# Optimization experiments

Hardware: AMD Instinct MI355X
Metric: run time of the kernel (lower is better)

The kernel has to match this reference:

```python
import jax, jax.numpy as jnp
import numpy as np
from jax import lax

EPS = 1e-5
C, H, W, G = 512, 32, 32, 32


def instance_norm(x):
    # torch InstanceNorm2d: affine=False, biased variance over (H,W)
    mu = x.mean(axis=(2, 3), keepdims=True)
    var = ((x - mu) ** 2).mean(axis=(2, 3), keepdims=True)
    return (x - mu) / jnp.sqrt(var + EPS)


def conv2d(x, w, stride=1, padding=0, groups=1, lhs_dilation=None):
    return lax.conv_general_dilated(
        x, w, (stride, stride), [(padding, padding)] * 2,
        lhs_dilation=lhs_dilation, feature_group_count=groups,
        dimension_numbers=('NCHW', 'OIHW', 'NCHW'))


def leaky_relu(x):
    return jnp.where(x >= 0, x, 0.2 * x)


def unfold(img, k, s):
    # img: (C,H,W) -> (nH*nW, C, k, k); matches torch unfold(1,k,s).unfold(2,k,s)
    c, h, w = img.shape
    nH = (h - k) // s + 1
    nW = (w - k) // s + 1
    rows = []
    for i in range(k):
        cols = [img[:, i:i + s * (nH - 1) + 1:s, j:j + s * (nW - 1) + 1:s] for j in range(k)]
        rows.append(jnp.stack(cols, axis=-1))  # (C,nH,nW,k)
    p = jnp.stack(rows, axis=-2)  # (C,nH,nW,k,k)
    return p.transpose(1, 2, 0, 3, 4).reshape(nH * nW, c, k, k)


def ral(bg, fg, rate=2, ksize=3, scale=10.0):
    # Region Affinity Layer (contextual-attention style), batch = 1
    b, c, h, w = fg.shape
    fh, fw = h // rate, w // rate
    # bilinear downsample by exactly 2 (half-pixel) == 2x2 average pooling
    fg_small = fg.reshape(b, c, fh, rate, fw, rate).mean(axis=(3, 5))
    bk = 2 * rate
    bg_patches = unfold(jnp.pad(bg, ((0, 0), (0, 0), (1, 1), (1, 1)))[0], bk, rate)      # (256,C,4,4)
    fg_patches = unfold(jnp.pad(fg_small, ((0, 0), (0, 0), (1, 1), (1, 1)))[0], ksize, 1)  # (256,C,3,3)
    norm = jnp.sqrt((fg_patches ** 2).sum(axis=(1, 2, 3), keepdims=True))
    fgp_n = fg_patches / jnp.maximum(norm, 1e-4)
    score = conv2d(fg_small, fgp_n, padding=1)        # (1,256,16,16)
    attn = jax.nn.softmax(score * scale, axis=1)
    # conv_transpose2d(attn, bg_patches, stride=rate, padding=1) via lhs dilation
    w_t = jnp.flip(bg_patches, axis=(-2, -1)).transpose(1, 0, 2, 3)  # (C,256,4,4)
    return conv2d(attn, w_t, padding=bk - 2, lhs_dilation=(rate, rate)) / 4.0  # (1,C,32,32)


def forward(x, gus, w_sk3, b_sk3, w_sk5, b_sk5, w_sk7, b_sk7,
            w_fc, b_fc, w_fc0, b_fc0, w_fc1, b_fc1, w_fc2, b_fc2, w_down, w_fuse):
    # ---- SKConv (M=3 branches: k=3/5/7, groups=32) ----
    feas = []
    for wgt, bias, pad in ((w_sk3, b_sk3, 1), (w_sk5, b_sk5, 2), (w_sk7, b_sk7, 3)):
        f = conv2d(x, wgt, padding=pad, groups=G) + bias[None, :, None, None]
        feas.append(jax.nn.relu(instance_norm(f)))
    feas = jnp.stack(feas, axis=1)                # (B,3,C,H,W)
    fea_s = feas.sum(axis=1).mean(axis=(2, 3))    # (B,C) global pool
    fea_z = fea_s @ w_fc.T + b_fc                 # (B,32)
    att = jnp.stack([fea_z @ w_fc0.T + b_fc0,
                     fea_z @ w_fc1.T + b_fc1,
                     fea_z @ w_fc2.T + b_fc2], axis=1)  # (B,3,C)
    att = jax.nn.softmax(att, axis=1)[..., None, None]
    out_32 = (feas * att).sum(axis=1)             # (1,C,32,32)
    out_res = out_32
    out_32 = ral(out_32, out_32)
    b, c, h, w = out_32.shape
    # ---- gaussian-weighted broadcast sum: (P,H,W)x(C,H,W)->(P,C)->raw reshape ----
    gus_out = jnp.einsum('pxy,cxy->pc', gus, out_32[0]).reshape(b, c, h, w)
    # ---- CSA patch correlation ----
    csa2_in = jax.nn.sigmoid(out_32)
    p_fff = unfold(jnp.pad(out_32, ((0, 0), (0, 0), (1, 1), (1, 1)))[0], 3, 1)    # (1024,C,3,3)
    p_f = unfold(jnp.pad(csa2_in, ((0, 0), (0, 0), (1, 1), (1, 1)))[0], 3, 1)     # (1024,C,3,3)
    p_conv = unfold(csa2_in[0], 1, 1)                                             # (1024,C,1,1)
    csa_a = (p_conv * p_f).mean(axis=1)                                           # (1024,3,3)
    csa_a = jax.nn.softmax(csa_a.reshape(h * w, 9), axis=1).reshape(h * w, 1, 3, 3)
    out_csa = (csa_a * p_fff).sum(axis=(-2, -1)).reshape(b, c, h, w)
    # ---- fuse ----
    z = jnp.concatenate([gus_out, out_csa], axis=1)       # (1,1024,32,32)
    z = leaky_relu(instance_norm(conv2d(z, w_down)))
    z = jnp.concatenate([z, out_res], axis=1)             # (1,1024,32,32)
    return leaky_relu(instance_norm(conv2d(z, w_fuse)))   # (1,512,32,32)


def _gaussian_buffer():
    # util.gussin(1.5): gaussian centered at every grid position of a 32x32 map
    v = 1.5
    r = np.arange(32)
    i, k, x, y = np.meshgrid(r, r, r, r, indexing='ij')
    g = np.exp(-((x - i) ** 2 + (y - k) ** 2) / (2 * v * v)) / (2 * np.pi * v * v)
    return jnp.asarray(g.reshape(32 * 32, 32, 32), dtype=jnp.float32)


def setup_inputs():
    key = jax.random.key(0)
    ks = jax.random.split(key, 12)
    s = 0.02
    return {
        'x': jax.random.normal(ks[0], (1, C, H, W), jnp.float32),
        'gus': _gaussian_buffer(),
        'w_sk3': jax.random.normal(ks[1], (C, C // G, 3, 3), jnp.float32) * s,
        'b_sk3': jnp.zeros((C,), jnp.float32),
        'w_sk5': jax.random.normal(ks[2], (C, C // G, 5, 5), jnp.float32) * s,
        'b_sk5': jnp.zeros((C,), jnp.float32),
        'w_sk7': jax.random.normal(ks[3], (C, C // G, 7, 7), jnp.float32) * s,
        'b_sk7': jnp.zeros((C,), jnp.float32),
        'w_fc': jax.random.normal(ks[4], (32, C), jnp.float32) * s,
        'b_fc': jnp.zeros((32,), jnp.float32),
        'w_fc0': jax.random.normal(ks[5], (C, 32), jnp.float32) * s,
        'b_fc0': jnp.zeros((C,), jnp.float32),
        'w_fc1': jax.random.normal(ks[6], (C, 32), jnp.float32) * s,
        'b_fc1': jnp.zeros((C,), jnp.float32),
        'w_fc2': jax.random.normal(ks[7], (C, 32), jnp.float32) * s,
        'b_fc2': jnp.zeros((C,), jnp.float32),
        'w_down': jax.random.normal(ks[8], (512, 1024, 1, 1), jnp.float32) * s,
        'w_fuse': jax.random.normal(ks[9], (512, 1024, 1, 1), jnp.float32) * s,
    }


def reference(x, gus, w_sk3, b_sk3, w_sk5, b_sk5, w_sk7, b_sk7, w_fc, b_fc,
              w_fc0, b_fc0, w_fc1, b_fc1, w_fc2, b_fc2, w_down, w_fuse):
    return forward(x, gus, w_sk3, b_sk3, w_sk5, b_sk5, w_sk7, b_sk7,
                   w_fc, b_fc, w_fc0, b_fc0, w_fc1, b_fc1, w_fc2, b_fc2,
                   w_down, w_fuse)
```

## Files before the change

kernel.cpp:

```cpp
#include <hip/hip_runtime.h>
#include <math.h>

#define EPSN 1e-5f

typedef __attribute__((ext_vector_type(8))) short bf16x8;
typedef __attribute__((ext_vector_type(4))) float f32x4;

__device__ __forceinline__ ushort f2bf(float f) {
  unsigned u = __float_as_uint(f);
  unsigned r = (u + 0x7fff + ((u >> 16) & 1)) >> 16;
  return (ushort)r;
}

__device__ __forceinline__ void breduce2(float& a, float& b, float* lds) {
#pragma unroll
  for (int o = 32; o > 0; o >>= 1) {
    a += __shfl_down(a, o);
    b += __shfl_down(b, o);
  }
  int lane = threadIdx.x & 63, wid = threadIdx.x >> 6;
  __syncthreads();
  if (lane == 0) { lds[wid] = a; lds[4 + wid] = b; }
  __syncthreads();
  a = lds[0] + lds[1] + lds[2] + lds[3];
  b = lds[4] + lds[5] + lds[6] + lds[7];
}

__device__ __forceinline__ float breduce_sum(float v, float* lds) {
#pragma unroll
  for (int o = 32; o > 0; o >>= 1) v += __shfl_down(v, o);
  int lane = threadIdx.x & 63, wid = threadIdx.x >> 6;
  __syncthreads();
  if (lane == 0) lds[wid] = v;
  __syncthreads();
  return lds[0] + lds[1] + lds[2] + lds[3];
}

__device__ __forceinline__ float breduce_max(float v, float* lds) {
#pragma unroll
  for (int o = 32; o > 0; o >>= 1) v = fmaxf(v, __shfl_down(v, o));
  int lane = threadIdx.x & 63, wid = threadIdx.x >> 6;
  __syncthreads();
  if (lane == 0) lds[wid] = v;
  __syncthreads();
  return fmaxf(fmaxf(lds[0], lds[1]), fmaxf(lds[2], lds[3]));
}

__global__ void pre_kernel(const float* __restrict__ gus,
                           const float* __restrict__ wdown,
                           const float* __restrict__ wfuse,
                           ushort* __restrict__ gus_bf,
                           ushort* __restrict__ wdown_bf,
                           ushort* __restrict__ wfuse_bf,
                           ushort* __restrict__ resd) {
  int bid = blockIdx.x, tid = threadIdx.x;
  if (bid < 2048) {
    int i = bid * 1024 + tid * 4;
    const float* src; ushort* dst; int off;
    if (i < 1048576) { src = gus; dst = gus_bf; off = i; }
    else if (i < 1572864) { src = wdown; dst = wdown_bf; off = i - 1048576; }
    else { src = wfuse; dst = wfuse_bf; off = i - 1572864; }
    float4 v = *(const float4*)&src[off];
    ushort4 o = {f2bf(v.x), f2bf(v.y), f2bf(v.z), f2bf(v.w)};
    *(ushort4*)&dst[off] = o;
  } else {
    int t8 = (bid - 2048) * 256 + tid;
    uint4 z = {0u, 0u, 0u, 0u};
#pragma unroll
    for (int k = 0; k < 4; ++k) *(uint4*)&resd[(size_t)(t8 + k * 65536) * 8] = z;
  }
}

__device__ __forceinline__ void finish3(float a[2][4], float bv, int m, int c,
                                        int y0, int xb, float* feas,
                                        float* bmean, float* red) {
  int tid = threadIdx.x, lane = tid & 63, wid = tid >> 6, pr = wid >> 1;
  float s = 0.f, ss = 0.f;
#pragma unroll
  for (int rr = 0; rr < 2; ++rr)
#pragma unroll
    for (int px = 0; px < 4; ++px) {
      a[rr][px] += bv;
      s += a[rr][px];
      ss += a[rr][px] * a[rr][px];
    }
#pragma unroll
  for (int o = 32; o > 0; o >>= 1) {
    s += __shfl_down(s, o);
    ss += __shfl_down(ss, o);
  }
  __syncthreads();
  if (lane == 0) { red[wid] = s; red[4 + wid] = ss; }
  __syncthreads();
  s = red[2 * pr] + red[2 * pr + 1];
  ss = red[4 + 2 * pr] + red[4 + 2 * pr + 1];
  float mean = s * (1.f / 1024.f);
  float var = ss * (1.f / 1024.f) - mean * mean;
  float inv = rsqrtf(var + EPSN);
  float rs = 0.f;
#pragma unroll
  for (int rr = 0; rr < 2; ++rr) {
    float4 o4;
    float* ov = (float*)&o4;
#pragma unroll
    for (int px = 0; px < 4; ++px) {
      float v = (a[rr][px] - mean) * inv;
      v = v > 0.f ? v : 0.f;
      ov[px] = v;
      rs += v;
    }
    *(float4*)&feas[(size_t)(m * 512 + c) * 1024 + (y0 + rr) * 32 + xb] = o4;
  }
#pragma unroll
  for (int o = 32; o > 0; o >>= 1) rs += __shfl_down(rs, o);
  __syncthreads();
  if (lane == 0) red[wid] = rs;
  __syncthreads();
  if ((tid & 127) == 0)
    bmean[m * 512 + c] = (red[2 * pr] + red[2 * pr + 1]) * (1.f / 1024.f);
}

__global__ __launch_bounds__(256) void sk_all5(
    const float* __restrict__ x, const float* __restrict__ w3,
    const float* __restrict__ b3, const float* __restrict__ w5,
    const float* __restrict__ b5, const float* __restrict__ w7,
    const float* __restrict__ b7, float* __restrict__ feas,
    float* __restrict__ bmean) {
  __shared__ float chanp[8 * 1536];
  __shared__ float ws7p[2 * 16 * 56];
  __shared__ float ws5p[2 * 16 * 40];
  __shared__ float ws3p[2 * 16 * 12];
  __shared__ float red[8];
  int bid = blockIdx.x, tid = threadIdx.x;
  int c0 = bid * 2, g = c0 >> 4;
  for (int i = tid; i < 8 * 1536; i += 256) chanp[i] = 0.f;
  for (int i = tid; i < 1792; i += 256) {
    int cw = i / 896, rem = i - cw * 896;
    int ic = rem / 56, t = rem - ic * 56, r = t >> 3, k = t & 7;
    ws7p[i] = (r < 7 && k < 7) ? w7[(c0 + cw) * 784 + ic * 49 + r * 7 + k] : 0.f;
  }
  for (int i = tid; i < 1280; i += 256) {
    int cw = i / 640, rem = i - cw * 640;
    int ic = rem / 40, t = rem - ic * 40, r = t >> 3, k = t & 7;
    ws5p[i] = (r < 5 && k < 5) ? w5[(c0 + cw) * 400 + ic * 25 + r * 5 + k] : 0.f;
  }
  for (int i = tid; i < 384; i += 256) {
    int cw = i / 192, rem = i - cw * 192;
    int ic = rem / 12, t = rem - ic * 12, r = t >> 2, k = t & 3;
    ws3p[i] = (k < 3) ? w3[(c0 + cw) * 144 + ic * 9 + r * 3 + k] : 0.f;
  }
  int ch = tid >> 7;
  int idx = tid & 127;
  int y0 = (idx >> 3) * 2, xb = (idx & 7) * 4;
  float a7[2][4] = {}, a5[2][4] = {}, a3[2][4] = {};
  int srow = tid >> 3, scol = (tid & 7) * 4;
  for (int half = 0; half < 2; ++half) {
    __syncthreads();
#pragma unroll
    for (int j = 0; j < 8; ++j) {
      float4 xv = *(const float4*)&x[(size_t)(g * 16 + half * 8 + j) * 1024 + tid * 4];
      *(float4*)&chanp[j * 1536 + srow * 48 + 4 + scol] = xv;
    }
    __syncthreads();
    for (int cc = 0; cc < 8; ++cc) {
      int ic = half * 8 + cc;
      float sg[8][12];
#pragma unroll
      for (int s = 0; s < 8; ++s) {
        int r = y0 - 3 + s;
        if ((unsigned)r < 32u) {
          const float* rp = &chanp[cc * 1536 + r * 48 + xb];
          float4 q0 = *(const float4*)rp;
          float4 q1 = *(const float4*)(rp + 4);
          float4 q2 = *(const float4*)(rp + 8);
          sg[s][0] = q0.x; sg[s][1] = q0.y; sg[s][2] = q0.z; sg[s][3] = q0.w;
          sg[s][4] = q1.x; sg[s][5] = q1.y; sg[s][6] = q1.z; sg[s][7] = q1.w;
          sg[s][8] = q2.x; sg[s][9] = q2.y; sg[s][10] = q2.z; sg[s][11] = q2.w;
        } else {
#pragma unroll
          for (int t = 0; t < 12; ++t) sg[s][t] = 0.f;
        }
      }
      const float* W7 = &ws7p[ch * 896 + ic * 56];
      const float* W5 = &ws5p[ch * 640 + ic * 40];
      const float* W3 = &ws3p[ch * 192 + ic * 12];
#pragma unroll
      for (int dy = 0; dy < 7; ++dy) {
        float4 wa = *(const float4*)(W7 + dy * 8);
        float4 wb = *(const float4*)(W7 + dy * 8 + 4);
        float wv[7] = {wa.x, wa.y, wa.z, wa.w, wb.x, wb.y, wb.z};
#pragma unroll
        for (int kx = 0; kx < 7; ++kx)
#pragma unroll
          for (int px = 0; px < 4; ++px) {
            a7[0][px] += sg[dy][px + kx + 1] * wv[kx];
            a7[1][px] += sg[dy + 1][px + kx + 1] * wv[kx];
          }
      }
#pragma unroll
      for (int d5 = 0; d5 < 5; ++d5) {
        float4 va = *(const float4*)(W5 + d5 * 8);
        float wv[5] = {va.x, va.y, va.z, va.w, W5[d5 * 8 + 4]};
#pragma unroll
        for (int kx = 0; kx < 5; ++kx)
#pragma unroll
          for (int px = 0; px < 4; ++px) {
            a5[0][px] += sg[d5 + 1][px + kx + 2] * wv[kx];
            a5[1][px] += sg[d5 + 2][px + kx + 2] * wv[kx];
          }
      }
#pragma unroll
      for (int d3 = 0; d3 < 3; ++d3) {
        float4 ta = *(const float4*)(W3 + d3 * 4);
        float wv[3] = {ta.x, ta.y, ta.z};
#pragma unroll
        for (int kx = 0; kx < 3; ++kx)
#pragma unroll
          for (int px = 0; px < 4; ++px) {
            a3[0][px] += sg[d3 + 2][px + kx + 3] * wv[kx];
            a3[1][px] += sg[d3 + 3][px + kx + 3] * wv[kx];
          }
      }
    }
  }
  int c = c0 + ch;
  finish3(a3, b3[c], 0, c, y0, xb, feas, bmean, red);
  finish3(a5, b5[c], 1, c, y0, xb, feas, bmean, red);
  finish3(a7, b7[c], 2, c, y0, xb, feas, bmean, red);
}

__global__ __launch_bounds__(256) void blend_fc(
    const float* __restrict__ feas, const float* __restrict__ bmean,
    const float* __restrict__ wfc, const float* __restrict__ bfc,
    const float* __restrict__ w0, const float* __restrict__ b0,
    const float* __restrict__ w1, const float* __restrict__ b1,
    const float* __restrict__ w2, const float* __restrict__ b2,
    float* __restrict__ res, ushort* __restrict__ Zt2,
    ushort* __restrict__ resd) {
  __shared__ float sfea[512];
  __shared__ float zpart[8][32];
  __shared__ float zz[32];
  __shared__ float lv[3][32];
  __shared__ float attb[3][32];
  __shared__ float tile[32][33];
  int tid = threadIdx.x;
  int pb = blockIdx.x * 32, cb = blockIdx.y * 32;
  for (int c = tid; c < 512; c += 256)
    sfea[c] = bmean[c] + bmean[512 + c] + bmean[1024 + c];
  __syncthreads();
  {
    int j = tid & 31, seg = tid >> 5;
    float p = 0.f;
    for (int c = seg * 64; c < seg * 64 + 64; ++c) p += sfea[c] * wfc[j * 512 + c];
    zpart[seg][j] = p;
  }
  __syncthreads();
  if (tid < 32) {
    float d = bfc[tid];
#pragma unroll
    for (int s = 0; s < 8; ++s) d += zpart[s][tid];
    zz[tid] = d;
  }
  __syncthreads();
  if (tid < 96) {
    int m = tid >> 5, cl = tid & 31;
    const float* wm = (m == 0) ? w0 : (m == 1) ? w1 : w2;
    const float* bm = (m == 0) ? b0 : (m == 1) ? b1 : b2;
    float l = bm[cb + cl];
#pragma unroll
    for (int j = 0; j < 32; ++j) l += zz[j] * wm[(cb + cl) * 32 + j];
    lv[m][cl] = l;
  }
  __syncthreads();
  if (tid < 32) {
    float l0 = lv[0][tid], l1 = lv[1][tid], l2 = lv[2][tid];
    float mx = fmaxf(l0, fmaxf(l1, l2));
    float e0 = expf(l0 - mx), e1 = expf(l1 - mx), e2 = expf(l2 - mx);
    float inv = 1.f / (e0 + e1 + e2);
    attb[0][tid] = e0 * inv; attb[1][tid] = e1 * inv; attb[2][tid] = e2 * inv;
  }
  __syncthreads();
  int tx = tid & 31, ty = tid >> 5;
  int pos = pb + tx;
  int yy = pos >> 5, xx = pos & 31;
  int ki0 = (yy + 1) & 1, pi0 = (yy + 1 - ki0) >> 1;
  int kj0 = (xx + 1) & 1, pj0 = (xx + 1 - kj0) >> 1;
#pragma unroll
  for (int r = 0; r < 4; ++r) {
    int cl = ty + r * 8;
    int c = cb + cl;
    float v = feas[c * 1024 + pos] * attb[0][cl] +
              feas[(512 + c) * 1024 + pos] * attb[1][cl] +
              feas[(1024 + c) * 1024 + pos] * attb[2][cl];
    res[c * 1024 + pos] = v;
    tile[cl][tx] = v;
    ushort bv16 = f2bf(v);
#pragma unroll
    for (int ai = 0; ai < 2; ++ai) {
      int ki = ki0 + 2 * ai, pi = pi0 - ai;
      if ((unsigned)pi >= 16u) continue;
#pragma unroll
      for (int aj = 0; aj < 2; ++aj) {
        int kj = kj0 + 2 * aj, pj = pj0 - aj;
        if ((unsigned)pj >= 16u) continue;
        resd[((size_t)(ki * 4 + kj) << 17) + (size_t)c * 256 + pi * 16 + pj] = bv16;
      }
    }
  }
  __syncthreads();
#pragma unroll
  for (int r = 0; r < 4; ++r) {
    int pl = ty + r * 8;
    Zt2[(size_t)(pb + pl) * 1024 + 512 + cb + tx] = f2bf(tile[tx][pl]);
  }
}

__global__ __launch_bounds__(256) void gram_part2(const float* __restrict__ res,
                                                  float* __restrict__ Apart) {
  __shared__ float ch[4][324];
  int tid = threadIdx.x;
  int qb = blockIdx.x * 64, pb = blockIdx.y * 64;
  int kc = blockIdx.z;
  int tx = tid & 15, ty = tid >> 4;
  for (int i = tid; i < 4 * 324; i += 256) ((float*)ch)[i] = 0.f;
  int pi = (pb + ty * 4) >> 4, pj = (pb + ty * 4) & 15;
  int qi = (qb + tx * 4) >> 4, qj = (qb + tx * 4) & 15;
  int lane = tid & 63, wv = tid >> 6;
  int sr = lane >> 2, sc = (lane & 3) * 4;
  float acc[4][4] = {};
  for (int c0 = kc * 16; c0 < kc * 16 + 16; c0 += 4) {
    __syncthreads();
    {
      const float* src = res + (size_t)(c0 + wv) * 1024 + (2 * sr) * 32 + 2 * sc;
      float4 r0a = *(const float4*)src;
      float4 r0b = *(const float4*)(src + 4);
      float4 r1a = *(const float4*)(src + 32);
      float4 r1b = *(const float4*)(src + 36);
      float* dst = &ch[wv][(sr + 1) * 18 + sc + 1];
      dst[0] = 0.25f * (r0a.x + r0a.y + r1a.x + r1a.y);
      dst[1] = 0.25f * (r0a.z + r0a.w + r1a.z + r1a.w);
      dst[2] = 0.25f * (r0b.x + r0b.y + r1b.x + r1b.y);
      dst[3] = 0.25f * (r0b.z + r0b.w + r1b.z + r1b.w);
    }
    __syncthreads();
#pragma unroll
    for (int cc = 0; cc < 4; ++cc) {
      float ps[3][6], qs[3][6];
#pragma unroll
      for (int u = 0; u < 3; ++u) {
        const float* pr = &ch[cc][(pi + u) * 18 + pj];
        const float* qr = &ch[cc][(qi + u) * 18 + qj];
#pragma unroll
        for (int t = 0; t < 6; ++t) { ps[u][t] = pr[t]; qs[u][t] = qr[t]; }
      }
#pragma unroll
      for (int u = 0; u < 3; ++u)
#pragma unroll
        for (int v = 0; v < 3; ++v)
#pragma unroll
          for (int i = 0; i < 4; ++i)
#pragma unroll
            for (int j = 0; j < 4; ++j)
              acc[i][j] += ps[u][v + i] * qs[u][v + j];
    }
  }
#pragma unroll
  for (int i = 0; i < 4; ++i) {
    float4 o4 = {acc[i][0], acc[i][1], acc[i][2], acc[i][3]};
    *(float4*)&Apart[(size_t)kc * 65536 + (pb + ty * 4 + i) * 256 + qb + tx * 4] = o4;
  }
}

__global__ __launch_bounds__(256) void attn_soft3(const float* __restrict__ Apart,
                                                  ushort* __restrict__ attnT) {
  __shared__ float red[8];
  int q = blockIdx.x, t = threadIdx.x;
  float d = 0.f, s = 0.f;
#pragma unroll
  for (int k = 0; k < 32; ++k) {
    d += Apart[(size_t)k * 65536 + t * 257];
    s += Apart[(size_t)k * 65536 + q * 256 + t];
  }
  float invn = 10.f / fmaxf(sqrtf(fmaxf(d, 0.f)), 1e-4f);
  float v = s * invn;
  float mx = breduce_max(v, red);
  float e = expf(v - mx);
  float sm = breduce_sum(e, red);
  attnT[q * 256 + t] = f2bf(e / sm);
}

__global__ __launch_bounds__(256) void mfma_tconv(const ushort* __restrict__ attnT,
                                                  const ushort* __restrict__ resd,
                                                  float* __restrict__ T) {
  int tid = threadIdx.x;
  int wv = tid >> 6, lane = tid & 63;
  int quad = lane >> 4, m16 = lane & 15;
  int nb = blockIdx.x * 64, qb = blockIdx.y * 64;
  int b = blockIdx.z;
  const ushort* Ap = attnT + (size_t)(qb + wv * 16 + m16) * 256 + quad * 8;
  const ushort* Bp = resd + (size_t)b * 131072 + (size_t)(nb + m16) * 256 + quad * 8;
  f32x4 ac0 = {0.f, 0.f, 0.f, 0.f}, ac1 = ac0, ac2 = ac0, ac3 = ac0;
#pragma unroll 2
  for (int k0 = 0; k0 < 256; k0 += 32) {
    bf16x8 af = *(const bf16x8*)(Ap + k0);
    bf16x8 b0 = *(const bf16x8*)(Bp + k0);
    bf16x8 b1 = *(const bf16x8*)(Bp + 16 * 256 + k0);
    bf16x8 b2 = *(const bf16x8*)(Bp + 32 * 256 + k0);
    bf16x8 b3 = *(const bf16x8*)(Bp + 48 * 256 + k0);
    ac0 = __builtin_amdgcn_mfma_f32_16x16x32_bf16(af, b0, ac0, 0, 0, 0);
    ac1 = __builtin_amdgcn_mfma_f32_16x16x32_bf16(af, b1, ac1, 0, 0, 0);
    ac2 = __builtin_amdgcn_mfma_f32_16x16x32_bf16(af, b2, ac2, 0, 0, 0);
    ac3 = __builtin_amdgcn_mfma_f32_16x16x32_bf16(af, b3, ac3, 0, 0, 0);
  }
  int row = qb + wv * 16 + quad * 4;
  float* Cb = T + (size_t)b * 131072;
  f32x4 accs[4] = {ac0, ac1, ac2, ac3};
#pragma unroll
  for (int nt = 0; nt < 4; ++nt)
#pragma unroll
    for (int r = 0; r < 4; ++r)
      Cb[(size_t)(row + r) * 512 + nb + nt * 16 + m16] = accs[nt][r];
}

__global__ __launch_bounds__(256) void tcomb2(const float* __restrict__ T,
                                              float* __restrict__ orlt,
                                              float* __restrict__ sigt,
                                              ushort* __restrict__ orlT) {
  __shared__ float tl[32][33];
  int nb = blockIdx.x * 32, cb = blockIdx.y * 32;
  int tx = threadIdx.x & 31, ty = threadIdx.x >> 5;
#pragma unroll
  for (int r = 0; r < 4; ++r) {
    int nl = ty + r * 8;
    int n = nb + nl, c = cb + tx;
    int y = n >> 5, x = n & 31;
    int i0 = (y + 1) >> 1, ki0 = (y + 1) & 1;
    int j0 = (x + 1) >> 1, kj0 = (x + 1) & 1;
    float sum = 0.f;
#pragma unroll
    for (int iy = 0; iy < 2; ++iy) {
      int i = i0 - iy, ki = ki0 + 2 * iy;
      if ((unsigned)i >= 16u) continue;
#pragma unroll
      for (int ix = 0; ix < 2; ++ix) {
        int j = j0 - ix, kj = kj0 + 2 * ix;
        if ((unsigned)j >= 16u) continue;
        sum += T[((ki * 4 + kj) * 256 + i * 16 + j) * 512 + c];
      }
    }
    float v = sum * 0.25f;
    orlt[n * 512 + c] = v;
    sigt[n * 512 + c] = 1.f / (1.f + expf(-v));
    tl[nl][tx] = v;
  }
  __syncthreads();
#pragma unroll
  for (int r = 0; r < 4; ++r) {
    int cl = ty + r * 8;
    orlT[(size_t)(cb + cl) * 1024 + nb + tx] = f2bf(tl[tx][cl]);
  }
}

__global__ __launch_bounds__(256) void gus_csa(
    const ushort* __restrict__ gus_bf, const ushort* __restrict__ orlT,
    const float* __restrict__ sigt, const float* __restrict__ orlt,
    ushort* __restrict__ Zt) {
  __shared__ float red[8];
  __shared__ float a9s[9];
  int tid = threadIdx.x;
  if (blockIdx.x < 128) {
    const int K = 1024;
    int wv = tid >> 6, lane = tid & 63;
    int quad = lane >> 4, m16 = lane & 15;
    int nb = (blockIdx.x & 7) * 64, mb = (blockIdx.x >> 3) * 64;
    const ushort* Ap = gus_bf + (size_t)(mb + wv * 16 + m16) * K + quad * 8;
    const ushort* Bp = orlT + (size_t)(nb + m16) * K + quad * 8;
    f32x4 ac0 = {0.f, 0.f, 0.f, 0.f}, ac1 = ac0, ac2 = ac0, ac3 = ac0;
#pragma unroll 2
    for (int k0 = 0; k0 < K; k0 += 32) {
      bf16x8 af = *(const bf16x8*)(Ap + k0);
      bf16x8 b0 = *(const bf16x8*)(Bp + k0);
      bf16x8 b1 = *(const bf16x8*)(Bp + (size_t)16 * K + k0);
      bf16x8 b2 = *(const bf16x8*)(Bp + (size_t)32 * K + k0);
      bf16x8 b3 = *(const bf16x8*)(Bp + (size_t)48 * K + k0);
      ac0 = __builtin_amdgcn_mfma_f32_16x16x32_bf16(af, b0, ac0, 0, 0, 0);
      ac1 = __builtin_amdgcn_mfma_f32_16x16x32_bf16(af, b1, ac1, 0, 0, 0);
      ac2 = __builtin_amdgcn_mfma_f32_16x16x32_bf16(af, b2, ac2, 0, 0, 0);
      ac3 = __builtin_amdgcn_mfma_f32_16x16x32_bf16(af, b3, ac3, 0, 0, 0);
    }
    int row = mb + wv * 16 + quad * 4;
    f32x4 accs[4] = {ac0, ac1, ac2, ac3};
#pragma unroll
    for (int nt = 0; nt < 4; ++nt) {
      int c = nb + nt * 16 + m16;
#pragma unroll
      for (int r = 0; r < 4; ++r) {
        int p = row + r;
        int pos = ((p & 1) << 9) + c;
        int kk = p >> 1;
        Zt[(size_t)pos * 1024 + kk] = f2bf(accs[nt][r]);
      }
    }
    return;
  }
  int n = blockIdx.x - 128;
  int ny = n >> 5, nx = n & 31;
  int c2 = tid * 2;
  float2 ctr = *(const float2*)&sigt[n * 512 + c2];
  float part[9];
#pragma unroll
  for (int u = 0; u < 3; ++u) {
    int yy = ny + u - 1;
#pragma unroll
    for (int v = 0; v < 3; ++v) {
      int xx = nx + v - 1;
      float2 nb2 = {0.f, 0.f};
      if ((unsigned)yy < 32u && (unsigned)xx < 32u)
        nb2 = *(const float2*)&sigt[(yy * 32 + xx) * 512 + c2];
      part[u * 3 + v] = ctr.x * nb2.x + ctr.y * nb2.y;
    }
  }
  float a[9];
#pragma unroll
  for (int t = 0; t < 9; ++t) a[t] = breduce_sum(part[t], red) * (1.f / 512.f);
  float mx = a[0];
#pragma unroll
  for (int t = 1; t < 9; ++t) mx = fmaxf(mx, a[t]);
  float sum = 0.f;
#pragma unroll
  for (int t = 0; t < 9; ++t) { a[t] = expf(a[t] - mx); sum += a[t]; }
  if (tid == 0) {
    float inv = 1.f / sum;
#pragma unroll
    for (int t = 0; t < 9; ++t) a9s[t] = a[t] * inv;
  }
  __syncthreads();
  float2 acc = {0.f, 0.f};
#pragma unroll
  for (int u = 0; u < 3; ++u) {
    int yy = ny + u - 1;
#pragma unroll
    for (int v = 0; v < 3; ++v) {
      int xx = nx + v - 1;
      if ((unsigned)yy < 32u && (unsigned)xx < 32u) {
        float w = a9s[u * 3 + v];
        float2 ov = *(const float2*)&orlt[(yy * 32 + xx) * 512 + c2];
        acc.x += w * ov.x;
        acc.y += w * ov.y;
      }
    }
  }
  int kk = 512 + (n >> 1);
  int pos0 = ((n & 1) << 9) + c2;
  Zt[(size_t)pos0 * 1024 + kk] = f2bf(acc.x);
  Zt[(size_t)(pos0 + 1) * 1024 + kk] = f2bf(acc.y);
}

__global__ __launch_bounds__(256) void mfma_gemm_ks(const ushort* __restrict__ A,
                                                    const ushort* __restrict__ Bt,
                                                    float* __restrict__ Cp,
                                                    int N) {
  const int KF = 1024;
  int tid = threadIdx.x;
  int wv = tid >> 6, lane = tid & 63;
  int quad = lane >> 4, m16 = lane & 15;
  int nb = blockIdx.x * 64, mb = blockIdx.y * 64;
  int kh = blockIdx.z;
  const ushort* Ap = A + (size_t)(mb + wv * 16 + m16) * KF + kh * 512 + quad * 8;
  const ushort* Bp = Bt + (size_t)(nb + m16) * KF + kh * 512 + quad * 8;
  f32x4 ac0 = {0.f, 0.f, 0.f, 0.f}, ac1 = ac0, ac2 = ac0, ac3 = ac0;
#pragma unroll 2
  for (int k0 = 0; k0 < 512; k0 += 32) {
    bf16x8 af = *(const bf16x8*)(Ap + k0);
    bf16x8 b0 = *(const bf16x8*)(Bp + k0);
    bf16x8 b1 = *(const bf16x8*)(Bp + (size_t)16 * KF + k0);
    bf16x8 b2 = *(const bf16x8*)(Bp + (size_t)32 * KF + k0);
    bf16x8 b3 = *(const bf16x8*)(Bp + (size_t)48 * KF + k0);
    ac0 = __builtin_amdgcn_mfma_f32_16x16x32_bf16(af, b0, ac0, 0, 0, 0);
    ac1 = __builtin_amdgcn_mfma_f32_16x16x32_bf16(af, b1, ac1, 0, 0, 0);
    ac2 = __builtin_amdgcn_mfma_f32_16x16x32_bf16(af, b2, ac2, 0, 0, 0);
    ac3 = __builtin_amdgcn_mfma_f32_16x16x32_bf16(af, b3, ac3, 0, 0, 0);
  }
  int row = mb + wv * 16 + quad * 4;
  float* C = Cp + (size_t)kh * 524288;
  f32x4 accs[4] = {ac0, ac1, ac2, ac3};
#pragma unroll
  for (int nt = 0; nt < 4; ++nt)
#pragma unroll
    for (int r = 0; r < 4; ++r)
      C[(size_t)(row + r) * N + nb + nt * 16 + m16] = accs[nt][r];
}

__global__ __launch_bounds__(256) void norm_down2(const float* __restrict__ ra,
                                                  ushort* __restrict__ Zt2) {
  __shared__ float red[8];
  int c = blockIdx.x, tid = threadIdx.x;
  float v[4];
  float s = 0.f, ss = 0.f;
#pragma unroll
  for (int r = 0; r < 4; ++r) {
    int i = c * 1024 + tid + r * 256;
    v[r] = ra[i] + ra[524288 + i];
    s += v[r];
    ss += v[r] * v[r];
  }
  breduce2(s, ss, red);
  float mean = s * (1.f / 1024.f);
  float var = ss * (1.f / 1024.f) - mean * mean;
  float inv = rsqrtf(var + EPSN);
#pragma unroll
  for (int r = 0; r < 4; ++r) {
    float t = (v[r] - mean) * inv;
    t = t >= 0.f ? t : 0.2f * t;
    Zt2[(size_t)(tid + r * 256) * 1024 + c] = f2bf(t);
  }
}

__global__ __launch_bounds__(256) void norm_leaky2(const float* __restrict__ ra,
                                                   float* __restrict__ out) {
  __shared__ float red[8];
  int c = blockIdx.x, tid = threadIdx.x;
  float v[4];
  float s = 0.f, ss = 0.f;
#pragma unroll
  for (int r = 0; r < 4; ++r) {
    int i = c * 1024 + tid + r * 256;
    v[r] = ra[i] + ra[524288 + i];
    s += v[r];
    ss += v[r] * v[r];
  }
  breduce2(s, ss, red);
  float mean = s * (1.f / 1024.f);
  float var = ss * (1.f / 1024.f) - mean * mean;
  float inv = rsqrtf(var + EPSN);
#pragma unroll
  for (int r = 0; r < 4; ++r) {
    float t = (v[r] - mean) * inv;
    out[c * 1024 + tid + r * 256] = t >= 0.f ? t : 0.2f * t;
  }
}

extern "C" void kernel_launch(void* const* d_in, const int* in_sizes, int n_in,
                              void* d_out, int out_size, void* d_ws, size_t ws_size,
                              hipStream_t stream) {
  const float* x = (const float*)d_in[0];
  const float* gus = (const float*)d_in[1];
  const float* w3 = (const float*)d_in[2];
  const float* b3 = (const float*)d_in[3];
  const float* w5 = (const float*)d_in[4];
  const float* b5 = (const float*)d_in[5];
  const float* w7 = (const float*)d_in[6];
  const float* b7 = (const float*)d_in[7];
  const float* wfc = (const float*)d_in[8];
  const float* bfc = (const float*)d_in[9];
  const float* w0 = (const float*)d_in[10];
  const float* b0 = (const float*)d_in[11];
  const float* w1 = (const float*)d_in[12];
  const float* b1 = (const float*)d_in[13];
  const float* w2 = (const float*)d_in[14];
  const float* b2 = (const float*)d_in[15];
  const float* wdown = (const float*)d_in[16];
  const float* wfuse = (const float*)d_in[17];

  float* ws = (float*)d_ws;
  float* feas = ws;
  float* rawP = feas + 524288;
  float* bmean = ws + 1572864;
  float* res = bmean + 1536;
  float* Zt2f = res + 524288;
  ushort* Zt2 = (ushort*)Zt2f;
  float* T = Zt2f + 524288;
  float* Apart = T;
  ushort* Zt = (ushort*)T;
  float* orlt = T + 2097152;
  float* sigt = orlt + 524288;
  ushort* orlT = (ushort*)(sigt + 524288);
  ushort* attnT = (ushort*)(sigt + 786432);
  ushort* gus_bf = (ushort*)(sigt + 819200);
  ushort* wdown_bf = (ushort*)(sigt + 1343488);
  ushort* wfuse_bf = (ushort*)(sigt + 1605632);
  ushort* resd = (ushort*)(sigt + 1867776);

  pre_kernel<<<2304, 256, 0, stream>>>(gus, wdown, wfuse, gus_bf, wdown_bf,
                                       wfuse_bf, resd);
  sk_all5<<<256, 256, 0, stream>>>(x, w3, b3, w5, b5, w7, b7, feas, bmean);
  blend_fc<<<dim3(32, 16), 256, 0, stream>>>(feas, bmean, wfc, bfc, w0, b0, w1,
                                             b1, w2, b2, res, Zt2, resd);
  gram_part2<<<dim3(4, 4, 32), 256, 0, stream>>>(res, Apart);
  attn_soft3<<<256, 256, 0, stream>>>(Apart, attnT);
  mfma_tconv<<<dim3(8, 4, 16), 256, 0, stream>>>(attnT, resd, T);
  tcomb2<<<dim3(32, 16), 256, 0, stream>>>(T, orlt, sigt, orlT);
  gus_csa<<<1152, 256, 0, stream>>>(gus_bf, orlT, sigt, orlt, Zt);
  mfma_gemm_ks<<<dim3(16, 8, 2), 256, 0, stream>>>(wdown_bf, Zt, rawP, 1024);
  norm_down2<<<512, 256, 0, stream>>>(rawP, Zt2);
  mfma_gemm_ks<<<dim3(16, 8, 2), 256, 0, stream>>>(wfuse_bf, Zt2, rawP, 1024);
  norm_leaky2<<<512, 256, 0, stream>>>(rawP, (float*)d_out);
}
```

Measured before the change: 259.9 us.

## Rewrite grouped SK convolutions as bf16 MFMA implicit GEMM with separate norm pass

Replaces the scalar FP32 grouped 3x3/5x5/7x7 convolution kernel with an implicit-GEMM kernel that packs weights and input halo into bf16 LDS tiles and uses 16x16x32 bf16 MFMA instructions. Instance norm, ReLU and channel mean now run in a separate kernel that reads raw conv outputs from workspace. The conv biases are dropped because instance norm cancels a per-channel constant. The aim is to cut the FP32 FMA cost of the convolutions, at the price of bf16 precision loss, an extra launch, and a round trip of the raw outputs through global memory.

```diff
diff --git a/kernel.cpp b/kernel.cpp
--- a/kernel.cpp
+++ b/kernel.cpp
@@ -71,162 +71,124 @@
   }
 }
 
-__device__ __forceinline__ void finish3(float a[2][4], float bv, int m, int c,
-                                        int y0, int xb, float* feas,
-                                        float* bmean, float* red) {
-  int tid = threadIdx.x, lane = tid & 63, wid = tid >> 6, pr = wid >> 1;
+__global__ __launch_bounds__(256) void sk_mfma(const float* __restrict__ x,
+                                               const float* __restrict__ w3,
+                                               const float* __restrict__ w5,
+                                               const float* __restrict__ w7,
+                                               float* __restrict__ feasRaw) {
+  __shared__ ushort xg[10 * 38 * 24];
+  __shared__ ushort Apk[43 * 32 * 16];
+  int bid = blockIdx.x, tid = threadIdx.x;
+  int g = bid >> 3, sl = bid & 7, y0 = sl * 4;
+  for (int i = tid; i < 4560; i += 256) ((uint*)xg)[i] = 0u;
+  for (int i = tid; i < 22016; i += 256) {
+    int p = i >> 9;
+    int r5 = i & 511;
+    int quad = r5 >> 7, m16 = (r5 >> 3) & 15, j = i & 7;
+    int k = quad * 8 + j, tp = k >> 4, ic = k & 15;
+    float val = 0.f;
+    if (p < 25) {
+      int t = 2 * p + tp;
+      if (t < 49) val = w7[(size_t)(g * 16 + m16) * 784 + ic * 49 + t];
+    } else if (p < 38) {
+      int t = 2 * (p - 25) + tp;
+      if (t < 25) val = w5[(size_t)(g * 16 + m16) * 400 + ic * 25 + t];
+    } else {
+      int t = 2 * (p - 38) + tp;
+      if (t < 9) val = w3[(size_t)(g * 16 + m16) * 144 + ic * 9 + t];
+    }
+    Apk[i] = f2bf(val);
+  }
+  __syncthreads();
+  for (int i = tid; i < 5120; i += 256) {
+    int lr = i >> 9, ic = (i >> 5) & 15, xc = i & 31;
+    int y = y0 + lr - 3;
+    if ((unsigned)y < 32u)
+      xg[(lr * 38 + xc + 3) * 24 + ic] =
+          f2bf(x[(size_t)(g * 16 + ic) * 1024 + y * 32 + xc]);
+  }
+  __syncthreads();
+  int wv = tid >> 6, lane = tid & 63, quad = lane >> 4, m16 = lane & 15;
+  int qh = (quad & 1) * 8, tp = quad >> 1;
+  f32x4 acc[2][3] = {};
+  for (int p = 0; p < 25; ++p) {
+    bf16x8 af = *(const bf16x8*)&Apk[(p * 4 + quad) * 128 + m16 * 8];
+    int t = 2 * p + tp;
+    if (t > 48) t = 48;
+    int ky = t / 7, kx = t - ky * 7;
+#pragma unroll
+    for (int ti = 0; ti < 2; ++ti) {
+      int T = wv + ti * 4, tl = T >> 1, x0c = (T & 1) * 16;
+      bf16x8 bf = *(const bf16x8*)&xg[((tl + ky) * 38 + x0c + m16 + kx) * 24 + qh];
+      acc[ti][2] = __builtin_amdgcn_mfma_f32_16x16x32_bf16(af, bf, acc[ti][2], 0, 0, 0);
+    }
+  }
+  for (int p = 0; p < 13; ++p) {
+    bf16x8 af = *(const bf16x8*)&Apk[((p + 25) * 4 + quad) * 128 + m16 * 8];
+    int t = 2 * p + tp;
+    if (t > 24) t = 24;
+    int ky = t / 5, kx = t - ky * 5;
+#pragma unroll
+    for (int ti = 0; ti < 2; ++ti) {
+      int T = wv + ti * 4, tl = T >> 1, x0c = (T & 1) * 16;
+      bf16x8 bf =
+          *(const bf16x8*)&xg[((tl + ky + 1) * 38 + x0c + m16 + kx + 1) * 24 + qh];
+      acc[ti][1] = __builtin_amdgcn_mfma_f32_16x16x32_bf16(af, bf, acc[ti][1], 0, 0, 0);
+    }
+  }
+  for (int p = 0; p < 5; ++p) {
+    bf16x8 af = *(const bf16x8*)&Apk[((p + 38) * 4 + quad) * 128 + m16 * 8];
+    int t = 2 * p + tp;
+    if (t > 8) t = 8;
+    int ky = t / 3, kx = t - ky * 3;
+#pragma unroll
+    for (int ti = 0; ti < 2; ++ti) {
+      int T = wv + ti * 4, tl = T >> 1, x0c = (T & 1) * 16;
+      bf16x8 bf =
+          *(const bf16x8*)&xg[((tl + ky + 2) * 38 + x0c + m16 + kx + 2) * 24 + qh];
+      acc[ti][0] = __builtin_amdgcn_mfma_f32_16x16x32_bf16(af, bf, acc[ti][0], 0, 0, 0);
+    }
+  }
+  int cb = g * 16 + quad * 4;
+#pragma unroll
+  for (int ti = 0; ti < 2; ++ti) {
+    int T = wv + ti * 4, tl = T >> 1, x0c = (T & 1) * 16;
+    int pos = (y0 + tl) * 32 + x0c + m16;
+#pragma unroll
+    for (int br = 0; br < 3; ++br)
+#pragma unroll
+      for (int r = 0; r < 4; ++r)
+        feasRaw[(size_t)(br * 512 + cb + r) * 1024 + pos] = acc[ti][br][r];
+  }
+}
+
+__global__ __launch_bounds__(256) void sk_norm(const float* __restrict__ raw,
+                                               float* __restrict__ feas,
+                                               float* __restrict__ bmean) {
+  __shared__ float red[8];
+  int mc = blockIdx.x, tid = threadIdx.x;
+  float v[4];
   float s = 0.f, ss = 0.f;
 #pragma unroll
-  for (int rr = 0; rr < 2; ++rr)
-#pragma unroll
-    for (int px = 0; px < 4; ++px) {
-      a[rr][px] += bv;
-      s += a[rr][px];
-      ss += a[rr][px] * a[rr][px];
-    }
-#pragma unroll
-  for (int o = 32; o > 0; o >>= 1) {
-    s += __shfl_down(s, o);
-    ss += __shfl_down(ss, o);
-  }
-  __syncthreads();
-  if (lane == 0) { red[wid] = s; red[4 + wid] = ss; }
-  __syncthreads();
-  s = red[2 * pr] + red[2 * pr + 1];
-  ss = red[4 + 2 * pr] + red[4 + 2 * pr + 1];
+  for (int r = 0; r < 4; ++r) {
+    v[r] = raw[(size_t)mc * 1024 + tid + r * 256];
+    s += v[r];
+    ss += v[r] * v[r];
+  }
+  breduce2(s, ss, red);
   float mean = s * (1.f / 1024.f);
   float var = ss * (1.f / 1024.f) - mean * mean;
   float inv = rsqrtf(var + EPSN);
   float rs = 0.f;
 #pragma unroll
-  for (int rr = 0; rr < 2; ++rr) {
-    float4 o4;
-    float* ov = (float*)&o4;
-#pragma unroll
-    for (int px = 0; px < 4; ++px) {
-      float v = (a[rr][px] - mean) * inv;
-      v = v > 0.f ? v : 0.f;
-      ov[px] = v;
-      rs += v;
-    }
-    *(float4*)&feas[(size_t)(m * 512 + c) * 1024 + (y0 + rr) * 32 + xb] = o4;
-  }
-#pragma unroll
-  for (int o = 32; o > 0; o >>= 1) rs += __shfl_down(rs, o);
-  __syncthreads();
-  if (lane == 0) red[wid] = rs;
-  __syncthreads();
-  if ((tid & 127) == 0)
-    bmean[m * 512 + c] = (red[2 * pr] + red[2 * pr + 1]) * (1.f / 1024.f);
-}
-
-__global__ __launch_bounds__(256) void sk_all5(
-    const float* __restrict__ x, const float* __restrict__ w3,
-    const float* __restrict__ b3, const float* __restrict__ w5,
-    const float* __restrict__ b5, const float* __restrict__ w7,
-    const float* __restrict__ b7, float* __restrict__ feas,
-    float* __restrict__ bmean) {
-  __shared__ float chanp[8 * 1536];
-  __shared__ float ws7p[2 * 16 * 56];
-  __shared__ float ws5p[2 * 16 * 40];
-  __shared__ float ws3p[2 * 16 * 12];
-  __shared__ float red[8];
-  int bid = blockIdx.x, tid = threadIdx.x;
-  int c0 = bid * 2, g = c0 >> 4;
-  for (int i = tid; i < 8 * 1536; i += 256) chanp[i] = 0.f;
-  for (int i = tid; i < 1792; i += 256) {
-    int cw = i / 896, rem = i - cw * 896;
-    int ic = rem / 56, t = rem - ic * 56, r = t >> 3, k = t & 7;
-    ws7p[i] = (r < 7 && k < 7) ? w7[(c0 + cw) * 784 + ic * 49 + r * 7 + k] : 0.f;
-  }
-  for (int i = tid; i < 1280; i += 256) {
-    int cw = i / 640, rem = i - cw * 640;
-    int ic = rem / 40, t = rem - ic * 40, r = t >> 3, k = t & 7;
-    ws5p[i] = (r < 5 && k < 5) ? w5[(c0 + cw) * 400 + ic * 25 + r * 5 + k] : 0.f;
-  }
-  for (int i = tid; i < 384; i += 256) {
-    int cw = i / 192, rem = i - cw * 192;
-    int ic = rem / 12, t = rem - ic * 12, r = t >> 2, k = t & 3;
-    ws3p[i] = (k < 3) ? w3[(c0 + cw) * 144 + ic * 9 + r * 3 + k] : 0.f;
-  }
-  int ch = tid >> 7;
-  int idx = tid & 127;
-  int y0 = (idx >> 3) * 2, xb = (idx & 7) * 4;
-  float a7[2][4] = {}, a5[2][4] = {}, a3[2][4] = {};
-  int srow = tid >> 3, scol = (tid & 7) * 4;
-  for (int half = 0; half < 2; ++half) {
-    __syncthreads();
-#pragma unroll
-    for (int j = 0; j < 8; ++j) {
-      float4 xv = *(const float4*)&x[(size_t)(g * 16 + half * 8 + j) * 1024 + tid * 4];
-      *(float4*)&chanp[j * 1536 + srow * 48 + 4 + scol] = xv;
-    }
-    __syncthreads();
-    for (int cc = 0; cc < 8; ++cc) {
-      int ic = half * 8 + cc;
-      float sg[8][12];
-#pragma unroll
-      for (int s = 0; s < 8; ++s) {
-        int r = y0 - 3 + s;
-        if ((unsigned)r < 32u) {
-          const float* rp = &chanp[cc * 1536 + r * 48 + xb];
-          float4 q0 = *(const float4*)rp;
-          float4 q1 = *(const float4*)(rp + 4);
-          float4 q2 = *(const float4*)(rp + 8);
-          sg[s][0] = q0.x; sg[s][1] = q0.y; sg[s][2] = q0.z; sg[s][3] = q0.w;
-          sg[s][4] = q1.x; sg[s][5] = q1.y; sg[s][6] = q1.z; sg[s][7] = q1.w;
-          sg[s][8] = q2.x; sg[s][9] = q2.y; sg[s][10] = q2.z; sg[s][11] = q2.w;
-        } else {
-#pragma unroll
-          for (int t = 0; t < 12; ++t) sg[s][t] = 0.f;
-        }
-      }
-      const float* W7 = &ws7p[ch * 896 + ic * 56];
-      const float* W5 = &ws5p[ch * 640 + ic * 40];
-      const float* W3 = &ws3p[ch * 192 + ic * 12];
-#pragma unroll
-      for (int dy = 0; dy < 7; ++dy) {
-        float4 wa = *(const float4*)(W7 + dy * 8);
-        float4 wb = *(const float4*)(W7 + dy * 8 + 4);
-        float wv[7] = {wa.x, wa.y, wa.z, wa.w, wb.x, wb.y, wb.z};
-#pragma unroll
-        for (int kx = 0; kx < 7; ++kx)
-#pragma unroll
-          for (int px = 0; px < 4; ++px) {
-            a7[0][px] += sg[dy][px + kx + 1] * wv[kx];
-            a7[1][px] += sg[dy + 1][px + kx + 1] * wv[kx];
-          }
-      }
-#pragma unroll
-      for (int d5 = 0; d5 < 5; ++d5) {
-        float4 va = *(const float4*)(W5 + d5 * 8);
-        float wv[5] = {va.x, va.y, va.z, va.w, W5[d5 * 8 + 4]};
-#pragma unroll
-        for (int kx = 0; kx < 5; ++kx)
-#pragma unroll
-          for (int px = 0; px < 4; ++px) {
-            a5[0][px] += sg[d5 + 1][px + kx + 2] * wv[kx];
-            a5[1][px] += sg[d5 + 2][px + kx + 2] * wv[kx];
-          }
-      }
-#pragma unroll
-      for (int d3 = 0; d3 < 3; ++d3) {
-        float4 ta = *(const float4*)(W3 + d3 * 4);
-        float wv[3] = {ta.x, ta.y, ta.z};
-#pragma unroll
-        for (int kx = 0; kx < 3; ++kx)
-#pragma unroll
-          for (int px = 0; px < 4; ++px) {
-            a3[0][px] += sg[d3 + 2][px + kx + 3] * wv[kx];
-            a3[1][px] += sg[d3 + 3][px + kx + 3] * wv[kx];
-          }
-      }
-    }
-  }
-  int c = c0 + ch;
-  finish3(a3, b3[c], 0, c, y0, xb, feas, bmean, red);
-  finish3(a5, b5[c], 1, c, y0, xb, feas, bmean, red);
-  finish3(a7, b7[c], 2, c, y0, xb, feas, bmean, red);
+  for (int r = 0; r < 4; ++r) {
+    float t = (v[r] - mean) * inv;
+    t = t > 0.f ? t : 0.f;
+    feas[(size_t)mc * 1024 + tid + r * 256] = t;
+    rs += t;
+  }
+  float tot = breduce_sum(rs, red);
+  if (tid == 0) bmean[mc] = tot * (1.f / 1024.f);
 }
 
 __global__ __launch_bounds__(256) void blend_fc(
@@ -646,11 +608,8 @@
   const float* x = (const float*)d_in[0];
   const float* gus = (const float*)d_in[1];
   const float* w3 = (const float*)d_in[2];
-  const float* b3 = (const float*)d_in[3];
   const float* w5 = (const float*)d_in[4];
-  const float* b5 = (const float*)d_in[5];
   const float* w7 = (const float*)d_in[6];
-  const float* b7 = (const float*)d_in[7];
   const float* wfc = (const float*)d_in[8];
   const float* bfc = (const float*)d_in[9];
   const float* w0 = (const float*)d_in[10];
@@ -670,6 +629,7 @@
   float* Zt2f = res + 524288;
   ushort* Zt2 = (ushort*)Zt2f;
   float* T = Zt2f + 524288;
+  float* feasRaw = T;
   float* Apart = T;
   ushort* Zt = (ushort*)T;
   float* orlt = T + 2097152;
@@ -683,7 +643,8 @@
 
   pre_kernel<<<2304, 256, 0, stream>>>(gus, wdown, wfuse, gus_bf, wdown_bf,
                                        wfuse_bf, resd);
-  sk_all5<<<256, 256, 0, stream>>>(x, w3, b3, w5, b5, w7, b7, feas, bmean);
+  sk_mfma<<<256, 256, 0, stream>>>(x, w3, w5, w7, feasRaw);
+  sk_norm<<<1536, 256, 0, stream>>>(feasRaw, feas, bmean);
   blend_fc<<<dim3(32, 16), 256, 0, stream>>>(feas, bmean, wfc, bfc, w0, b0, w1,
                                              b1, w2, b2, res, Zt2, resd);
   gram_part2<<<dim3(4, 4, 32), 256, 0, stream>>>(res, Apart);
```

New measurement: 259.9 us. No clear change (-0.0%).
